# Kernel tuning notes

Measured on AMD Instinct MI355X. Metric: run time of the kernel, lower is better.

Reference implementation:

```python
import jax, jax.numpy as jnp
import numpy as np

N_NODES = 50000
NEG_SLOPE = 0.2
EPS = 1e-16


def _gat_layer(x, src, dst, W, a_src, a_dst, b, concat):
    """One PyG-style GATConv layer (eval mode, self-loops already in src/dst).
    x: [N, F_in], W: [F_in, H*C], a_src/a_dst: [H, C], b: [H*C] or [C].
    """
    H, C = a_src.shape
    N = x.shape[0]
    h = (x @ W).reshape(N, H, C)                      # [N, H, C]
    alpha_s = jnp.einsum('nhc,hc->nh', h, a_src)      # [N, H]
    alpha_d = jnp.einsum('nhc,hc->nh', h, a_dst)      # [N, H]
    e = alpha_s[src] + alpha_d[dst]                   # [E, H]
    e = jax.nn.leaky_relu(e, NEG_SLOPE)
    # segment softmax over edges grouped by destination node
    m = jax.ops.segment_max(e, dst, num_segments=N)   # [N, H]
    e = jnp.exp(e - m[dst])
    denom = jax.ops.segment_sum(e, dst, num_segments=N)
    alpha = e / (denom[dst] + EPS)                    # [E, H]
    msg = h[src] * alpha[:, :, None]                  # [E, H, C]
    out = jax.ops.segment_sum(msg, dst, num_segments=N)  # [N, H, C]
    if concat:
        out = out.reshape(N, H * C)
    else:
        out = out.mean(axis=1)
    return out + b


def setup_inputs() -> dict:
    key = jax.random.key(0)
    ks = jax.random.split(key, 16)
    N, E = N_NODES, 800000
    in_dim, hid, heads = 128, 64, 2
    x = jax.random.normal(ks[0], (N, in_dim), dtype=jnp.float32)
    edge_index = jax.random.randint(ks[1], (2, E), 0, N, dtype=jnp.int64)
    s = 0.1
    return {
        'x': x,
        'edge_index': edge_index,
        # layer 0: in_dim -> hid, heads
        'W0': s * jax.random.normal(ks[2], (in_dim, heads * hid), dtype=jnp.float32),
        'as0': s * jax.random.normal(ks[3], (heads, hid), dtype=jnp.float32),
        'ad0': s * jax.random.normal(ks[4], (heads, hid), dtype=jnp.float32),
        'b0': jnp.zeros((heads * hid,), dtype=jnp.float32),
        # layer 1: hid*heads -> hid, heads
        'W1': s * jax.random.normal(ks[5], (heads * hid, heads * hid), dtype=jnp.float32),
        'as1': s * jax.random.normal(ks[6], (heads, hid), dtype=jnp.float32),
        'ad1': s * jax.random.normal(ks[7], (heads, hid), dtype=jnp.float32),
        'b1': jnp.zeros((heads * hid,), dtype=jnp.float32),
        # layer 2: hid*heads -> hid, heads=1
        'W2': s * jax.random.normal(ks[8], (heads * hid, hid), dtype=jnp.float32),
        'as2': s * jax.random.normal(ks[9], (1, hid), dtype=jnp.float32),
        'ad2': s * jax.random.normal(ks[10], (1, hid), dtype=jnp.float32),
        'b2': jnp.zeros((hid,), dtype=jnp.float32),
    }


def reference(x, edge_index, W0, as0, ad0, b0, W1, as1, ad1, b1, W2, as2, ad2, b2):
    N = x.shape[0]
    # PyG GATConv default add_self_loops=True
    loop = jnp.arange(N, dtype=edge_index.dtype)
    src = jnp.concatenate([edge_index[0], loop])
    dst = jnp.concatenate([edge_index[1], loop])
    h = _gat_layer(x, src, dst, W0, as0, ad0, b0, concat=True)
    h = jax.nn.relu(h)
    h = _gat_layer(h, src, dst, W1, as1, ad1, b1, concat=True)
    h = jax.nn.relu(h)
    out = _gat_layer(h, src, dst, W2, as2, ad2, b2, concat=True)  # heads=1: concat == identity
    return out
```

## Files before the change

### kernel.cpp

```cpp
#include <hip/hip_runtime.h>
#include <hip/hip_fp16.h>

#define NEG_SLOPE 0.2f
#define EPSF 1e-16f

template<int BN, int HEADS, bool OUTH, typename XT>
__global__ __launch_bounds__(256) void gemm_fused(const XT* __restrict__ X,
                                                  const float* __restrict__ W,
                                                  const float* __restrict__ asrc,
                                                  const float* __restrict__ adst,
                                                  float* __restrict__ OutF,
                                                  __half* __restrict__ OutH,
                                                  float* __restrict__ AS,
                                                  float* __restrict__ AD, int N) {
    constexpr int BM = 64, BK = 32, K = 128;
    constexpr int TN = BN / 16;
    __shared__ float Xs[BM][BK + 4];
    __shared__ float Ws[BK][BN];
    const int tid = threadIdx.x;
    const int tx = tid & 15, ty = tid >> 4;
    const int row0 = blockIdx.x * BM;

    float acc[4][TN];
#pragma unroll
    for (int i = 0; i < 4; ++i)
#pragma unroll
        for (int j = 0; j < TN; ++j) acc[i][j] = 0.f;

    for (int kb = 0; kb < K; kb += BK) {
        __syncthreads();
        for (int idx = tid; idx < BK * (BN / 4); idx += 256) {
            int r = idx / (BN / 4), c4 = idx % (BN / 4);
            ((float4*)&Ws[r][0])[c4] = ((const float4*)&W[(size_t)(kb + r) * BN])[c4];
        }
        for (int t = tid; t < BM * (BK / 4); t += 256) {
            int r = t >> 3, c4 = t & 7;
            int gr = row0 + r;
            float f[4] = {0.f, 0.f, 0.f, 0.f};
            if (gr < N) {
                if constexpr (sizeof(XT) == 2) {
                    uint2 raw = *((const uint2*)&X[(size_t)gr * K + kb + c4 * 4]);
                    const __half2* hp = (const __half2*)&raw;
                    float2 f0 = __half22float2(hp[0]);
                    float2 f1 = __half22float2(hp[1]);
                    f[0] = f0.x; f[1] = f0.y; f[2] = f1.x; f[3] = f1.y;
                } else {
                    float4 v = *((const float4*)&X[(size_t)gr * K + kb + c4 * 4]);
                    f[0] = v.x; f[1] = v.y; f[2] = v.z; f[3] = v.w;
                }
            }
            Xs[r][c4 * 4 + 0] = f[0]; Xs[r][c4 * 4 + 1] = f[1];
            Xs[r][c4 * 4 + 2] = f[2]; Xs[r][c4 * 4 + 3] = f[3];
        }
        __syncthreads();
#pragma unroll
        for (int k = 0; k < BK; ++k) {
            float xr[4];
#pragma unroll
            for (int i = 0; i < 4; ++i) xr[i] = Xs[ty * 4 + i][k];
            float wv[TN];
#pragma unroll
            for (int j4 = 0; j4 < TN / 4; ++j4) {
                float4 w4 = ((float4*)&Ws[k][0])[tx * (TN / 4) + j4];
                wv[j4 * 4 + 0] = w4.x; wv[j4 * 4 + 1] = w4.y;
                wv[j4 * 4 + 2] = w4.z; wv[j4 * 4 + 3] = w4.w;
            }
#pragma unroll
            for (int i = 0; i < 4; ++i)
#pragma unroll
                for (int j = 0; j < TN; ++j) acc[i][j] = fmaf(xr[i], wv[j], acc[i][j]);
        }
    }

    float av[TN], dv[TN];
#pragma unroll
    for (int j = 0; j < TN; ++j) { av[j] = asrc[tx * TN + j]; dv[j] = adst[tx * TN + j]; }

#pragma unroll
    for (int i = 0; i < 4; ++i) {
        int gr = row0 + ty * 4 + i;
        if (gr >= N) continue;
        if (OUTH) {
            __half2 hp[TN / 2];
#pragma unroll
            for (int j2 = 0; j2 < TN / 2; ++j2)
                hp[j2] = __floats2half2_rn(acc[i][j2 * 2], acc[i][j2 * 2 + 1]);
            if (TN == 8)
                *((uint4*)&OutH[(size_t)gr * BN + tx * TN]) = *(uint4*)hp;
            else
                *((uint2*)&OutH[(size_t)gr * BN + tx * TN]) = *(uint2*)hp;
        } else {
#pragma unroll
            for (int j4 = 0; j4 < TN / 4; ++j4) {
                float4 o4 = make_float4(acc[i][j4 * 4 + 0], acc[i][j4 * 4 + 1],
                                        acc[i][j4 * 4 + 2], acc[i][j4 * 4 + 3]);
                *((float4*)&OutF[(size_t)gr * BN + tx * TN + j4 * 4]) = o4;
            }
        }
        float ps = 0.f, pd = 0.f;
#pragma unroll
        for (int j = 0; j < TN; ++j) { ps = fmaf(acc[i][j], av[j], ps); pd = fmaf(acc[i][j], dv[j], pd); }
        if (HEADS == 2) {
            for (int o = 1; o < 8; o <<= 1) { ps += __shfl_xor(ps, o, 64); pd += __shfl_xor(pd, o, 64); }
            if ((tx & 7) == 0) { AS[gr * 2 + (tx >> 3)] = ps; AD[gr * 2 + (tx >> 3)] = pd; }
        } else {
            for (int o = 1; o < 16; o <<= 1) { ps += __shfl_xor(ps, o, 64); pd += __shfl_xor(pd, o, 64); }
            if (tx == 0) { AS[gr] = ps; AD[gr] = pd; }
        }
    }
}

__global__ void zero_kernel(int* __restrict__ p, int n4) {
    int i = blockIdx.x * blockDim.x + threadIdx.x;
    if (i < n4) ((int4*)p)[i] = make_int4(0, 0, 0, 0);
}

__global__ void hist_kernel(const int* __restrict__ ei, int E_raw, int N,
                            int* __restrict__ cnt) {
    const int E = E_raw + N;
    for (int e = blockIdx.x * blockDim.x + threadIdx.x; e < E; e += gridDim.x * blockDim.x) {
        int d = (e < E_raw) ? ei[E_raw + e] : e - E_raw;
        atomicAdd(&cnt[d], 1);
    }
}

__global__ __launch_bounds__(256) void scan_block(const int* __restrict__ cnt,
                                                  int* __restrict__ offs,
                                                  int* __restrict__ bsum, int N) {
    __shared__ int wsum[4];
    const int i = blockIdx.x * 256 + threadIdx.x;
    const int lane = threadIdx.x & 63, w = threadIdx.x >> 6;
    int v = (i < N) ? cnt[i] : 0;
    int incl = v;
    for (int o = 1; o < 64; o <<= 1) {
        int t = __shfl_up(incl, o, 64);
        if (lane >= o) incl += t;
    }
    if (lane == 63) wsum[w] = incl;
    __syncthreads();
    int prefix = 0;
    for (int k = 0; k < w; ++k) prefix += wsum[k];
    if (i < N) offs[i] = prefix + incl - v;
    if (threadIdx.x == 255) bsum[blockIdx.x] = prefix + incl;
}

__global__ __launch_bounds__(256) void scan_bsum(int* __restrict__ bsum, int nb) {
    __shared__ int wsum[4];
    const int lane = threadIdx.x & 63, w = threadIdx.x >> 6;
    int v = (threadIdx.x < nb) ? bsum[threadIdx.x] : 0;
    int incl = v;
    for (int o = 1; o < 64; o <<= 1) {
        int t = __shfl_up(incl, o, 64);
        if (lane >= o) incl += t;
    }
    if (lane == 63) wsum[w] = incl;
    __syncthreads();
    int prefix = 0;
    for (int k = 0; k < w; ++k) prefix += wsum[k];
    if (threadIdx.x < nb) bsum[threadIdx.x] = prefix + incl - v;
}

__global__ void scan_add(int* __restrict__ offs, const int* __restrict__ bsum,
                         int N, int E) {
    const int i = blockIdx.x * 256 + threadIdx.x;
    if (i < N) offs[i] += bsum[blockIdx.x];
    if (i == 0) offs[N] = E;
}

__global__ void scatter_edges_part(const int* __restrict__ ei, int E_raw, int N,
                                   int* __restrict__ cnt,
                                   const int* __restrict__ offs,
                                   int* __restrict__ csr_src) {
    const int NPART = 8;
    const int part = blockIdx.x & (NPART - 1);
    const int gblocks = gridDim.x >> 3;
    const int grank = blockIdx.x >> 3;
    const int tid = grank * blockDim.x + threadIdx.x;
    const int nthr = gblocks * blockDim.x;
    const int E = E_raw + N;
    const int dlo = (int)(((long long)N * part) / NPART);
    const int dhi = (int)(((long long)N * (part + 1)) / NPART);
    for (int e = tid; e < E; e += nthr) {
        int d = (e < E_raw) ? ei[E_raw + e] : e - E_raw;
        if (d >= dlo && d < dhi) {
            int s = (e < E_raw) ? ei[e] : d;
            int old = atomicSub(&cnt[d], 1);
            csr_src[offs[d] + old - 1] = s;
        }
    }
}

__global__ __launch_bounds__(256) void gat_csr2(const int* __restrict__ offs,
                                                const int* __restrict__ csr_src,
                                                const float* __restrict__ AS,
                                                const float* __restrict__ AD,
                                                const __half* __restrict__ H,
                                                const float* __restrict__ bias,
                                                __half* __restrict__ Out,
                                                int N, int do_relu) {
    __shared__ int   sS[4][64];
    __shared__ float sP0[4][64];
    __shared__ float sP1[4][64];
    const int lane = threadIdx.x & 63;
    const int w = threadIdx.x >> 6;
    const int wid = (int)((blockIdx.x * blockDim.x + threadIdx.x) >> 6);
    const int nw = (int)((gridDim.x * blockDim.x) >> 6);
    const int c = lane & 15;
    const int slot = lane >> 4;
    const int myh = c >> 3;
    int* const sSw = &sS[w][0];
    const float* const myp = myh ? &sP1[w][0] : &sP0[w][0];
    const float4 bA = *(const float4*)&bias[8 * c];
    const float4 bB = *(const float4*)&bias[8 * c + 4];

    for (int n = wid; n < N; n += nw) {
        const int s0 = offs[n], s1 = offs[n + 1];
        const int deg = s1 - s0;
        const float2 adv = *(const float2*)&AD[(size_t)n * 2];
        float dn0 = 0.f, dn1 = 0.f, p0 = 0.f, p1 = 0.f;
        int sreg = 0;
        for (int i = s0 + lane; i < s1; i += 64) {
            int s = csr_src[i];
            float2 a2 = *(const float2*)&AS[(size_t)s * 2];
            float e0 = a2.x + adv.x, e1 = a2.y + adv.y;
            e0 = e0 > 0.f ? e0 : NEG_SLOPE * e0;
            e1 = e1 > 0.f ? e1 : NEG_SLOPE * e1;
            float pe0 = __expf(e0), pe1 = __expf(e1);
            dn0 += pe0; dn1 += pe1;
            if (i == s0 + lane) { sreg = s; p0 = pe0; p1 = pe1; }
        }
        for (int o = 1; o < 64; o <<= 1) {
            dn0 += __shfl_xor(dn0, o, 64);
            dn1 += __shfl_xor(dn1, o, 64);
        }
        const float myinv = 1.f / ((myh ? dn1 : dn0) + EPSF);

        float a[8];
#pragma unroll
        for (int j = 0; j < 8; ++j) a[j] = 0.f;
        if (deg <= 64) {
            sSw[lane] = sreg;
            sP0[w][lane] = p0;
            sP1[w][lane] = p1;
            const int npc = (deg + 3) >> 2;
            int t = 0;
            for (; t + 4 <= npc; t += 4) {
                int ss[4]; float pw[4]; uint4 hv[4];
#pragma unroll
                for (int k = 0; k < 4; ++k) {
                    int idx = 4 * (t + k) + slot;
                    ss[k] = sSw[idx];
                    pw[k] = myp[idx];
                }
#pragma unroll
                for (int k = 0; k < 4; ++k)
                    hv[k] = *(const uint4*)&H[(size_t)ss[k] * 128 + 8 * c];
#pragma unroll
                for (int k = 0; k < 4; ++k) {
                    const __half2* h2 = (const __half2*)&hv[k];
#pragma unroll
                    for (int j = 0; j < 4; ++j) {
                        float2 f = __half22float2(h2[j]);
                        a[2 * j]     = fmaf(f.x, pw[k], a[2 * j]);
                        a[2 * j + 1] = fmaf(f.y, pw[k], a[2 * j + 1]);
                    }
                }
            }
            for (; t < npc; ++t) {
                int idx = 4 * t + slot;
                int s = sSw[idx];
                float pw = myp[idx];
                uint4 hv = *(const uint4*)&H[(size_t)s * 128 + 8 * c];
                const __half2* h2 = (const __half2*)&hv;
#pragma unroll
                for (int j = 0; j < 4; ++j) {
                    float2 f = __half22float2(h2[j]);
                    a[2 * j]     = fmaf(f.x, pw, a[2 * j]);
                    a[2 * j + 1] = fmaf(f.y, pw, a[2 * j + 1]);
                }
            }
        } else {
            const float advh = myh ? adv.y : adv.x;
            for (int i = s0 + slot; i < s1; i += 4) {
                int s = csr_src[i];
                float e = AS[(size_t)s * 2 + myh] + advh;
                e = e > 0.f ? e : NEG_SLOPE * e;
                float pw = __expf(e);
                uint4 hv = *(const uint4*)&H[(size_t)s * 128 + 8 * c];
                const __half2* h2 = (const __half2*)&hv;
#pragma unroll
                for (int j = 0; j < 4; ++j) {
                    float2 f = __half22float2(h2[j]);
                    a[2 * j]     = fmaf(f.x, pw, a[2 * j]);
                    a[2 * j + 1] = fmaf(f.y, pw, a[2 * j + 1]);
                }
            }
        }
#pragma unroll
        for (int j = 0; j < 8; ++j) {
            a[j] += __shfl_xor(a[j], 16, 64);
            a[j] += __shfl_xor(a[j], 32, 64);
        }
        if (lane < 16) {
            float o[8];
            o[0] = a[0] * myinv + bA.x; o[1] = a[1] * myinv + bA.y;
            o[2] = a[2] * myinv + bA.z; o[3] = a[3] * myinv + bA.w;
            o[4] = a[4] * myinv + bB.x; o[5] = a[5] * myinv + bB.y;
            o[6] = a[6] * myinv + bB.z; o[7] = a[7] * myinv + bB.w;
            if (do_relu) {
#pragma unroll
                for (int j = 0; j < 8; ++j) o[j] = fmaxf(o[j], 0.f);
            }
            __half2 hp[4];
#pragma unroll
            for (int j = 0; j < 4; ++j) hp[j] = __floats2half2_rn(o[2 * j], o[2 * j + 1]);
            *(uint4*)&Out[(size_t)n * 128 + 8 * c] = *(uint4*)hp;
        }
    }
}

__global__ __launch_bounds__(256) void gat_csr1(const int* __restrict__ offs,
                                                const int* __restrict__ csr_src,
                                                const float* __restrict__ AS,
                                                const float* __restrict__ AD,
                                                const __half* __restrict__ H,
                                                const float* __restrict__ bias,
                                                float* __restrict__ Out,
                                                int N, int do_relu) {
    __shared__ int   sS[4][64];
    __shared__ float sP[4][64];
    const int lane = threadIdx.x & 63;
    const int w = threadIdx.x >> 6;
    const int wid = (int)((blockIdx.x * blockDim.x + threadIdx.x) >> 6);
    const int nw = (int)((gridDim.x * blockDim.x) >> 6);
    const int c = lane & 15;
    const int slot = lane >> 4;
    int* const sSw = &sS[w][0];
    float* const sPw = &sP[w][0];
    const float4 b4 = *(const float4*)&bias[4 * c];

    for (int n = wid; n < N; n += nw) {
        const int s0 = offs[n], s1 = offs[n + 1];
        const int deg = s1 - s0;
        const float adv0 = AD[n];
        float dn0 = 0.f, p0 = 0.f;
        int sreg = 0;
        for (int i = s0 + lane; i < s1; i += 64) {
            int s = csr_src[i];
            float e0 = AS[s] + adv0;
            e0 = e0 > 0.f ? e0 : NEG_SLOPE * e0;
            float pe0 = __expf(e0);
            dn0 += pe0;
            if (i == s0 + lane) { sreg = s; p0 = pe0; }
        }
        for (int o = 1; o < 64; o <<= 1) dn0 += __shfl_xor(dn0, o, 64);
        const float inv0 = 1.f / (dn0 + EPSF);

        float a[4];
#pragma unroll
        for (int j = 0; j < 4; ++j) a[j] = 0.f;
        if (deg <= 64) {
            sSw[lane] = sreg;
            sPw[lane] = p0;
            const int npc = (deg + 3) >> 2;
            int t = 0;
            for (; t + 4 <= npc; t += 4) {
                int ss[4]; float pw[4]; uint2 hv[4];
#pragma unroll
                for (int k = 0; k < 4; ++k) {
                    int idx = 4 * (t + k) + slot;
                    ss[k] = sSw[idx];
                    pw[k] = sPw[idx];
                }
#pragma unroll
                for (int k = 0; k < 4; ++k)
                    hv[k] = *(const uint2*)&H[(size_t)ss[k] * 64 + 4 * c];
#pragma unroll
                for (int k = 0; k < 4; ++k) {
                    const __half2* h2 = (const __half2*)&hv[k];
                    float2 f01 = __half22float2(h2[0]);
                    float2 f23 = __half22float2(h2[1]);
                    a[0] = fmaf(f01.x, pw[k], a[0]);
                    a[1] = fmaf(f01.y, pw[k], a[1]);
                    a[2] = fmaf(f23.x, pw[k], a[2]);
                    a[3] = fmaf(f23.y, pw[k], a[3]);
                }
            }
            for (; t < npc; ++t) {
                int idx = 4 * t + slot;
                int s = sSw[idx];
                float pw = sPw[idx];
                uint2 hv = *(const uint2*)&H[(size_t)s * 64 + 4 * c];
                const __half2* h2 = (const __half2*)&hv;
                float2 f01 = __half22float2(h2[0]);
                float2 f23 = __half22float2(h2[1]);
                a[0] = fmaf(f01.x, pw, a[0]);
                a[1] = fmaf(f01.y, pw, a[1]);
                a[2] = fmaf(f23.x, pw, a[2]);
                a[3] = fmaf(f23.y, pw, a[3]);
            }
        } else {
            for (int i = s0 + slot; i < s1; i += 4) {
                int s = csr_src[i];
                float e = AS[s] + adv0;
                e = e > 0.f ? e : NEG_SLOPE * e;
                float pw = __expf(e);
                uint2 hv = *(const uint2*)&H[(size_t)s * 64 + 4 * c];
                const __half2* h2 = (const __half2*)&hv;
                float2 f01 = __half22float2(h2[0]);
                float2 f23 = __half22float2(h2[1]);
                a[0] = fmaf(f01.x, pw, a[0]);
                a[1] = fmaf(f01.y, pw, a[1]);
                a[2] = fmaf(f23.x, pw, a[2]);
                a[3] = fmaf(f23.y, pw, a[3]);
            }
        }
#pragma unroll
        for (int j = 0; j < 4; ++j) {
            a[j] += __shfl_xor(a[j], 16, 64);
            a[j] += __shfl_xor(a[j], 32, 64);
        }
        if (lane < 16) {
            float4 o;
            o.x = a[0] * inv0 + b4.x;
            o.y = a[1] * inv0 + b4.y;
            o.z = a[2] * inv0 + b4.z;
            o.w = a[3] * inv0 + b4.w;
            if (do_relu) {
                o.x = fmaxf(o.x, 0.f); o.y = fmaxf(o.y, 0.f);
                o.z = fmaxf(o.z, 0.f); o.w = fmaxf(o.w, 0.f);
            }
            *(float4*)&Out[(size_t)n * 64 + 4 * c] = o;
        }
    }
}

extern "C" void kernel_launch(void* const* d_in, const int* in_sizes, int n_in,
                              void* d_out, int out_size, void* d_ws, size_t ws_size,
                              hipStream_t stream) {
    const float* x   = (const float*)d_in[0];
    const int*   ei  = (const int*)d_in[1];
    const float* W0  = (const float*)d_in[2];
    const float* as0 = (const float*)d_in[3];
    const float* ad0 = (const float*)d_in[4];
    const float* b0  = (const float*)d_in[5];
    const float* W1  = (const float*)d_in[6];
    const float* as1 = (const float*)d_in[7];
    const float* ad1 = (const float*)d_in[8];
    const float* b1  = (const float*)d_in[9];
    const float* W2  = (const float*)d_in[10];
    const float* as2 = (const float*)d_in[11];
    const float* ad2 = (const float*)d_in[12];
    const float* b2  = (const float*)d_in[13];

    const int N = in_sizes[0] / 128;
    const int E_raw = in_sizes[1] / 2;
    const int E = E_raw + N;

    char* ws = (char*)d_ws;
    size_t off = 0;
    auto alloc = [&](size_t bytes) {
        void* p = ws + off;
        off = (off + bytes + 255) & ~(size_t)255;
        return p;
    };
    __half* hh    = (__half*)alloc((size_t)N * 128 * 2);
    __half* obufh = (__half*)alloc((size_t)N * 128 * 2);
    float* asb  = (float*)alloc((size_t)N * 2 * 4);
    float* adb  = (float*)alloc((size_t)N * 2 * 4);
    int*   cnt  = (int*)alloc((size_t)(N + 4) * 4);
    int*   offs = (int*)alloc((size_t)(N + 1) * 4);
    int*   bsum = (int*)alloc(1024);
    int* csr_src = (int*)alloc((size_t)E * 4);
    (void)ws_size; (void)n_in; (void)out_size;

    const int nb = (N + 255) / 256;
    const int n4 = (N + 3) / 4;
    zero_kernel<<<(n4 + 255) / 256, 256, 0, stream>>>(cnt, n4);
    hist_kernel<<<2048, 256, 0, stream>>>(ei, E_raw, N, cnt);
    scan_block<<<nb, 256, 0, stream>>>(cnt, offs, bsum, N);
    scan_bsum<<<1, 256, 0, stream>>>(bsum, nb);
    scan_add<<<nb, 256, 0, stream>>>(offs, bsum, N, E);
    scatter_edges_part<<<2048, 256, 0, stream>>>(ei, E_raw, N, cnt, offs, csr_src);

    const int gemm_blocks = (N + 63) / 64;
    const int gat_blocks = 2048;

    gemm_fused<128, 2, true, float><<<gemm_blocks, 256, 0, stream>>>(x, W0, as0, ad0, nullptr, hh, asb, adb, N);
    gat_csr2<<<gat_blocks, 256, 0, stream>>>(offs, csr_src, asb, adb, hh, b0, obufh, N, 1);
    gemm_fused<128, 2, true, __half><<<gemm_blocks, 256, 0, stream>>>(obufh, W1, as1, ad1, nullptr, hh, asb, adb, N);
    gat_csr2<<<gat_blocks, 256, 0, stream>>>(offs, csr_src, asb, adb, hh, b1, obufh, N, 1);
    gemm_fused<64, 1, true, __half><<<gemm_blocks, 256, 0, stream>>>(obufh, W2, as2, ad2, nullptr, hh, asb, adb, N);
    gat_csr1<<<gat_blocks, 256, 0, stream>>>(offs, csr_src, asb, adb, hh, b2, (float*)d_out, N, 0);
}
```

Before: 275.2 us.

## Use MFMA fp16 GEMM for GAT projections and partition histogram atomics

Replaces the scalar FMA tiled GEMM with an MFMA 16x16x32 fp16 kernel that stages the transposed weights in shared memory as fp16, and adds a kernel that first converts the fp32 input features to fp16. The histogram kernel now splits blocks into eight destination-range partitions, so each block group only does atomics on its own slice of the count array. This trades more compute for less atomic contention. Risks include an extra conversion pass over x, fp16 rounding of inputs and weights, and scattered 2-byte output stores.

```diff
diff --git a/kernel.cpp b/kernel.cpp
--- a/kernel.cpp
+++ b/kernel.cpp
@@ -4,108 +4,98 @@
 #define NEG_SLOPE 0.2f
 #define EPSF 1e-16f
 
-template<int BN, int HEADS, bool OUTH, typename XT>
-__global__ __launch_bounds__(256) void gemm_fused(const XT* __restrict__ X,
-                                                  const float* __restrict__ W,
-                                                  const float* __restrict__ asrc,
-                                                  const float* __restrict__ adst,
-                                                  float* __restrict__ OutF,
-                                                  __half* __restrict__ OutH,
-                                                  float* __restrict__ AS,
-                                                  float* __restrict__ AD, int N) {
-    constexpr int BM = 64, BK = 32, K = 128;
-    constexpr int TN = BN / 16;
-    __shared__ float Xs[BM][BK + 4];
-    __shared__ float Ws[BK][BN];
+typedef _Float16 half8 __attribute__((ext_vector_type(8)));
+typedef float floatx4 __attribute__((ext_vector_type(4)));
+
+__global__ void to_half_kernel(const float* __restrict__ in, __half* __restrict__ out,
+                               int n8) {
+    int i = blockIdx.x * blockDim.x + threadIdx.x;
+    if (i < n8) {
+        float4 a = ((const float4*)in)[i * 2];
+        float4 b = ((const float4*)in)[i * 2 + 1];
+        __half2 hp[4];
+        hp[0] = __floats2half2_rn(a.x, a.y);
+        hp[1] = __floats2half2_rn(a.z, a.w);
+        hp[2] = __floats2half2_rn(b.x, b.y);
+        hp[3] = __floats2half2_rn(b.z, b.w);
+        ((uint4*)out)[i] = *(uint4*)hp;
+    }
+}
+
+template<int BN, int HEADS>
+__global__ __launch_bounds__(256) void gemm_mfma(const __half* __restrict__ X,
+                                                 const float* __restrict__ W,
+                                                 const float* __restrict__ asrc,
+                                                 const float* __restrict__ adst,
+                                                 __half* __restrict__ OutH,
+                                                 float* __restrict__ AS,
+                                                 float* __restrict__ AD, int N) {
+    constexpr int KP = 136;
+    constexpr int NF = BN / 16;
+    __shared__ _Float16 Wt[BN][KP];
     const int tid = threadIdx.x;
-    const int tx = tid & 15, ty = tid >> 4;
-    const int row0 = blockIdx.x * BM;
-
-    float acc[4][TN];
-#pragma unroll
-    for (int i = 0; i < 4; ++i)
-#pragma unroll
-        for (int j = 0; j < TN; ++j) acc[i][j] = 0.f;
-
-    for (int kb = 0; kb < K; kb += BK) {
-        __syncthreads();
-        for (int idx = tid; idx < BK * (BN / 4); idx += 256) {
-            int r = idx / (BN / 4), c4 = idx % (BN / 4);
-            ((float4*)&Ws[r][0])[c4] = ((const float4*)&W[(size_t)(kb + r) * BN])[c4];
-        }
-        for (int t = tid; t < BM * (BK / 4); t += 256) {
-            int r = t >> 3, c4 = t & 7;
-            int gr = row0 + r;
-            float f[4] = {0.f, 0.f, 0.f, 0.f};
-            if (gr < N) {
-                if constexpr (sizeof(XT) == 2) {
-                    uint2 raw = *((const uint2*)&X[(size_t)gr * K + kb + c4 * 4]);
-                    const __half2* hp = (const __half2*)&raw;
-                    float2 f0 = __half22float2(hp[0]);
-                    float2 f1 = __half22float2(hp[1]);
-                    f[0] = f0.x; f[1] = f0.y; f[2] = f1.x; f[3] = f1.y;
-                } else {
-                    float4 v = *((const float4*)&X[(size_t)gr * K + kb + c4 * 4]);
-                    f[0] = v.x; f[1] = v.y; f[2] = v.z; f[3] = v.w;
-                }
-            }
-            Xs[r][c4 * 4 + 0] = f[0]; Xs[r][c4 * 4 + 1] = f[1];
-            Xs[r][c4 * 4 + 2] = f[2]; Xs[r][c4 * 4 + 3] = f[3];
-        }
-        __syncthreads();
-#pragma unroll
-        for (int k = 0; k < BK; ++k) {
-            float xr[4];
-#pragma unroll
-            for (int i = 0; i < 4; ++i) xr[i] = Xs[ty * 4 + i][k];
-            float wv[TN];
-#pragma unroll
-            for (int j4 = 0; j4 < TN / 4; ++j4) {
-                float4 w4 = ((float4*)&Ws[k][0])[tx * (TN / 4) + j4];
-                wv[j4 * 4 + 0] = w4.x; wv[j4 * 4 + 1] = w4.y;
-                wv[j4 * 4 + 2] = w4.z; wv[j4 * 4 + 3] = w4.w;
-            }
-#pragma unroll
-            for (int i = 0; i < 4; ++i)
-#pragma unroll
-                for (int j = 0; j < TN; ++j) acc[i][j] = fmaf(xr[i], wv[j], acc[i][j]);
-        }
-    }
-
-    float av[TN], dv[TN];
-#pragma unroll
-    for (int j = 0; j < TN; ++j) { av[j] = asrc[tx * TN + j]; dv[j] = adst[tx * TN + j]; }
-
-#pragma unroll
-    for (int i = 0; i < 4; ++i) {
-        int gr = row0 + ty * 4 + i;
-        if (gr >= N) continue;
-        if (OUTH) {
-            __half2 hp[TN / 2];
-#pragma unroll
-            for (int j2 = 0; j2 < TN / 2; ++j2)
-                hp[j2] = __floats2half2_rn(acc[i][j2 * 2], acc[i][j2 * 2 + 1]);
-            if (TN == 8)
-                *((uint4*)&OutH[(size_t)gr * BN + tx * TN]) = *(uint4*)hp;
-            else
-                *((uint2*)&OutH[(size_t)gr * BN + tx * TN]) = *(uint2*)hp;
-        } else {
-#pragma unroll
-            for (int j4 = 0; j4 < TN / 4; ++j4) {
-                float4 o4 = make_float4(acc[i][j4 * 4 + 0], acc[i][j4 * 4 + 1],
-                                        acc[i][j4 * 4 + 2], acc[i][j4 * 4 + 3]);
-                *((float4*)&OutF[(size_t)gr * BN + tx * TN + j4 * 4]) = o4;
-            }
-        }
-        float ps = 0.f, pd = 0.f;
-#pragma unroll
-        for (int j = 0; j < TN; ++j) { ps = fmaf(acc[i][j], av[j], ps); pd = fmaf(acc[i][j], dv[j], pd); }
-        if (HEADS == 2) {
-            for (int o = 1; o < 8; o <<= 1) { ps += __shfl_xor(ps, o, 64); pd += __shfl_xor(pd, o, 64); }
-            if ((tx & 7) == 0) { AS[gr * 2 + (tx >> 3)] = ps; AD[gr * 2 + (tx >> 3)] = pd; }
-        } else {
-            for (int o = 1; o < 16; o <<= 1) { ps += __shfl_xor(ps, o, 64); pd += __shfl_xor(pd, o, 64); }
-            if (tx == 0) { AS[gr] = ps; AD[gr] = pd; }
+    const int wave = tid >> 6, lane = tid & 63;
+    const int r = lane & 15;
+    const int g = lane >> 4;
+    const int row0 = blockIdx.x * 64 + wave * 16;
+
+    for (int idx = tid; idx < 128 * (BN / 4); idx += 256) {
+        int k = idx / (BN / 4), n4 = idx % (BN / 4);
+        float4 w4 = *(const float4*)&W[(size_t)k * BN + n4 * 4];
+        Wt[n4 * 4 + 0][k] = (_Float16)w4.x;
+        Wt[n4 * 4 + 1][k] = (_Float16)w4.y;
+        Wt[n4 * 4 + 2][k] = (_Float16)w4.z;
+        Wt[n4 * 4 + 3][k] = (_Float16)w4.w;
+    }
+    __syncthreads();
+
+    const int arow = row0 + r;
+    const int arow_c = (arow < N) ? arow : (N - 1);
+
+    floatx4 acc[NF];
+#pragma unroll
+    for (int n = 0; n < NF; ++n) acc[n] = (floatx4)(0.f);
+
+#pragma unroll
+    for (int ks = 0; ks < 4; ++ks) {
+        half8 afrag = *(const half8*)&X[(size_t)arow_c * 128 + ks * 32 + g * 8];
+#pragma unroll
+        for (int n = 0; n < NF; ++n) {
+            half8 bfrag = *(const half8*)&Wt[n * 16 + r][ks * 32 + g * 8];
+            acc[n] = __builtin_amdgcn_mfma_f32_16x16x32_f16(afrag, bfrag, acc[n], 0, 0, 0);
+        }
+    }
+
+    float av[NF], dv[NF];
+#pragma unroll
+    for (int n = 0; n < NF; ++n) { av[n] = asrc[n * 16 + r]; dv[n] = adst[n * 16 + r]; }
+
+#pragma unroll
+    for (int reg = 0; reg < 4; ++reg) {
+        const int orow = row0 + g * 4 + reg;
+        if (orow >= N) continue;
+#pragma unroll
+        for (int n = 0; n < NF; ++n)
+            OutH[(size_t)orow * BN + n * 16 + r] = __float2half(acc[n][reg]);
+        float ps0 = 0.f, pd0 = 0.f, ps1 = 0.f, pd1 = 0.f;
+#pragma unroll
+        for (int n = 0; n < NF; ++n) {
+            float v = acc[n][reg];
+            if (HEADS == 2 && n >= NF / 2) { ps1 = fmaf(v, av[n], ps1); pd1 = fmaf(v, dv[n], pd1); }
+            else                           { ps0 = fmaf(v, av[n], ps0); pd0 = fmaf(v, dv[n], pd0); }
+        }
+#pragma unroll
+        for (int o = 1; o < 16; o <<= 1) {
+            ps0 += __shfl_xor(ps0, o, 64); pd0 += __shfl_xor(pd0, o, 64);
+            if (HEADS == 2) { ps1 += __shfl_xor(ps1, o, 64); pd1 += __shfl_xor(pd1, o, 64); }
+        }
+        if (r == 0) {
+            if (HEADS == 2) {
+                AS[orow * 2] = ps0; AS[orow * 2 + 1] = ps1;
+                AD[orow * 2] = pd0; AD[orow * 2 + 1] = pd1;
+            } else {
+                AS[orow] = ps0; AD[orow] = pd0;
+            }
         }
     }
 }
@@ -115,12 +105,20 @@
     if (i < n4) ((int4*)p)[i] = make_int4(0, 0, 0, 0);
 }
 
-__global__ void hist_kernel(const int* __restrict__ ei, int E_raw, int N,
-                            int* __restrict__ cnt) {
+__global__ void hist_part(const int* __restrict__ ei, int E_raw, int N,
+                          int* __restrict__ cnt) {
+    const int NPART = 8;
+    const int part = blockIdx.x & (NPART - 1);
+    const int gblocks = gridDim.x >> 3;
+    const int grank = blockIdx.x >> 3;
+    const int tid = grank * blockDim.x + threadIdx.x;
+    const int nthr = gblocks * blockDim.x;
     const int E = E_raw + N;
-    for (int e = blockIdx.x * blockDim.x + threadIdx.x; e < E; e += gridDim.x * blockDim.x) {
+    const int dlo = (int)(((long long)N * part) / NPART);
+    const int dhi = (int)(((long long)N * (part + 1)) / NPART);
+    for (int e = tid; e < E; e += nthr) {
         int d = (e < E_raw) ? ei[E_raw + e] : e - E_raw;
-        atomicAdd(&cnt[d], 1);
+        if (d >= dlo && d < dhi) atomicAdd(&cnt[d], 1);
     }
 }
 
@@ -464,6 +462,7 @@
         off = (off + bytes + 255) & ~(size_t)255;
         return p;
     };
+    __half* xh    = (__half*)alloc((size_t)N * 128 * 2);
     __half* hh    = (__half*)alloc((size_t)N * 128 * 2);
     __half* obufh = (__half*)alloc((size_t)N * 128 * 2);
     float* asb  = (float*)alloc((size_t)N * 2 * 4);
@@ -477,19 +476,22 @@
     const int nb = (N + 255) / 256;
     const int n4 = (N + 3) / 4;
     zero_kernel<<<(n4 + 255) / 256, 256, 0, stream>>>(cnt, n4);
-    hist_kernel<<<2048, 256, 0, stream>>>(ei, E_raw, N, cnt);
+    hist_part<<<2048, 256, 0, stream>>>(ei, E_raw, N, cnt);
     scan_block<<<nb, 256, 0, stream>>>(cnt, offs, bsum, N);
     scan_bsum<<<1, 256, 0, stream>>>(bsum, nb);
     scan_add<<<nb, 256, 0, stream>>>(offs, bsum, N, E);
     scatter_edges_part<<<2048, 256, 0, stream>>>(ei, E_raw, N, cnt, offs, csr_src);
 
+    const int n8 = N * 128 / 8;
+    to_half_kernel<<<(n8 + 255) / 256, 256, 0, stream>>>(x, xh, n8);
+
     const int gemm_blocks = (N + 63) / 64;
     const int gat_blocks = 2048;
 
-    gemm_fused<128, 2, true, float><<<gemm_blocks, 256, 0, stream>>>(x, W0, as0, ad0, nullptr, hh, asb, adb, N);
+    gemm_mfma<128, 2><<<gemm_blocks, 256, 0, stream>>>(xh, W0, as0, ad0, hh, asb, adb, N);
     gat_csr2<<<gat_blocks, 256, 0, stream>>>(offs, csr_src, asb, adb, hh, b0, obufh, N, 1);
-    gemm_fused<128, 2, true, __half><<<gemm_blocks, 256, 0, stream>>>(obufh, W1, as1, ad1, nullptr, hh, asb, adb, N);
+    gemm_mfma<128, 2><<<gemm_blocks, 256, 0, stream>>>(obufh, W1, as1, ad1, hh, asb, adb, N);
     gat_csr2<<<gat_blocks, 256, 0, stream>>>(offs, csr_src, asb, adb, hh, b1, obufh, N, 1);
-    gemm_fused<64, 1, true, __half><<<gemm_blocks, 256, 0, stream>>>(obufh, W2, as2, ad2, nullptr, hh, asb, adb, N);
+    gemm_mfma<64, 1><<<gemm_blocks, 256, 0, stream>>>(obufh, W2, as2, ad2, hh, asb, adb, N);
     gat_csr1<<<gat_blocks, 256, 0, stream>>>(offs, csr_src, asb, adb, hh, b2, (float*)d_out, N, 0);
 }
```

After: 257.2 us. -6.5%, faster.
